# Performance work log

Measured on AMD Instinct MI355X. Metric: run time of the kernel, lower is better.

## Reference

```python
import jax, jax.numpy as jnp
import numpy as np

NEG = -1e4      # BigBird additive mask value
LN_EPS = 1e-12  # BERT-style LayerNorm eps


def _bigbird_forward(xs_pad, mask, Wq, bq, Wk, bk, Wv, bv, Wo, bo, gamma, beta, rand_idx):
    b, n, hsz = xs_pad.shape
    H = rand_idx.shape[0]
    nb = rand_idx.shape[1] + 2          # one rand row per non-edge query block
    BS = n // nb                        # block size
    d = hsz // H
    r = rand_idx.shape[2]
    scale = 1.0 / np.sqrt(d).astype(np.float32)

    mf = mask.reshape(b, n).astype(xs_pad.dtype)   # (b,n) 1=token, 0=pad
    mb = mf.reshape(b, nb, BS)                     # blocked mask

    def proj(W, bias):
        return (xs_pad @ W + bias).reshape(b, n, H, d).transpose(0, 2, 1, 3)

    q = proj(Wq, bq) * scale            # (b,H,n,d)
    k = proj(Wk, bk)
    v = proj(Wv, bv)
    qb = q.reshape(b, H, nb, BS, d)
    kb = k.reshape(b, H, nb, BS, d)
    vb = v.reshape(b, H, nb, BS, d)

    # ---- global rows: first / last query block attend to all keys ----
    def full_row(qi):                   # qi: (b,H,BS,d)
        s = jnp.einsum('bhqd,bhkd->bhqk', qi, k) + (1.0 - mf)[:, None, None, :] * NEG
        return jnp.einsum('bhqk,bhkd->bhqd', jax.nn.softmax(s, axis=-1), v)

    ctx_first = full_row(qb[:, :, 0])
    ctx_last = full_row(qb[:, :, nb - 1])

    # ---- random key/value blocks: per-head, per-query-block gather ----
    hidx = jnp.arange(H)[:, None, None]
    rand_k = kb[:, hidx, rand_idx].reshape(b, H, nb - 2, r * BS, d)
    rand_v = vb[:, hidx, rand_idx].reshape(b, H, nb - 2, r * BS, d)
    rand_m = mb[:, rand_idx].reshape(b, H, nb - 2, r * BS)

    def sparse_row(qi, kc, vc, mc):     # kc:(b,H,K,d), mc:(b,H,K)
        s = jnp.einsum('bhqd,bhkd->bhqk', qi, kc) + (1.0 - mc)[:, :, None, :] * NEG
        return jnp.einsum('bhqk,bhkd->bhqd', jax.nn.softmax(s, axis=-1), vc)

    def gather_blocks(ids, ridx):
        kc = jnp.concatenate([kb[:, :, j] for j in ids] + [rand_k[:, :, ridx]], axis=2)
        vc = jnp.concatenate([vb[:, :, j] for j in ids] + [rand_v[:, :, ridx]], axis=2)
        mc = jnp.concatenate([jnp.broadcast_to(mb[:, None, j], (b, H, BS)) for j in ids]
                             + [rand_m[:, :, ridx]], axis=2)
        return kc, vc, mc

    # second / penultimate query blocks: window + globals + rand
    ctx_second = sparse_row(qb[:, :, 1], *gather_blocks([0, 1, 2, nb - 1], 0))
    ctx_penult = sparse_row(qb[:, :, nb - 2], *gather_blocks([nb - 3, nb - 2, nb - 1, 0], nb - 3))

    # ---- middle rows i in [2, nb-3]: 3-block sliding window + first/last global + r random ----
    nmid = nb - 4
    mid = jnp.arange(2, nb - 2)
    win = mid[:, None] + jnp.arange(-1, 2)[None, :]        # (nmid,3)
    k_win = kb[:, :, win].reshape(b, H, nmid, 3 * BS, d)
    v_win = vb[:, :, win].reshape(b, H, nmid, 3 * BS, d)
    m_win = jnp.broadcast_to(mb[:, win].reshape(b, 1, nmid, 3 * BS), (b, H, nmid, 3 * BS))

    def rep_glob(t):                     # (b,H,BS,...) -> (b,H,nmid,BS,...)
        return jnp.broadcast_to(t[:, :, None], (b, H, nmid) + t.shape[2:])

    k_mid = jnp.concatenate([k_win, rep_glob(kb[:, :, 0]), rep_glob(kb[:, :, nb - 1]),
                             rand_k[:, :, 1:nb - 3]], axis=3)
    v_mid = jnp.concatenate([v_win, rep_glob(vb[:, :, 0]), rep_glob(vb[:, :, nb - 1]),
                             rand_v[:, :, 1:nb - 3]], axis=3)
    m_first = jnp.broadcast_to(mb[:, None, None, 0], (b, H, nmid, BS))
    m_last = jnp.broadcast_to(mb[:, None, None, nb - 1], (b, H, nmid, BS))
    m_mid = jnp.concatenate([m_win, m_first, m_last, rand_m[:, :, 1:nb - 3]], axis=3)

    s_mid = jnp.einsum('bhmqd,bhmkd->bhmqk', qb[:, :, 2:nb - 2], k_mid) \
            + (1.0 - m_mid)[:, :, :, None, :] * NEG
    ctx_mid = jnp.einsum('bhmqk,bhmkd->bhmqd', jax.nn.softmax(s_mid, axis=-1), v_mid)

    ctx = jnp.concatenate([ctx_first[:, :, None], ctx_second[:, :, None], ctx_mid,
                           ctx_penult[:, :, None], ctx_last[:, :, None]], axis=2)
    ctx = ctx.reshape(b, H, n, d).transpose(0, 2, 1, 3).reshape(b, n, hsz)
    ctx = ctx * mf[:, :, None]           # from_mask on output rows

    # BigBirdSelfOutput: dense + residual + LayerNorm (dropout=0 / eval)
    y = ctx @ Wo + bo + xs_pad
    mu = y.mean(-1, keepdims=True)
    var = ((y - mu) ** 2).mean(-1, keepdims=True)
    return (y - mu) * jax.lax.rsqrt(var + LN_EPS) * gamma + beta


def setup_inputs() -> dict:
    key = jax.random.key(0)
    ks = jax.random.split(key, 6)
    B, N, HSZ, H, BS, R = 4, 4096, 1024, 16, 64, 3
    NB = N // BS
    init = lambda k, shp: jax.random.normal(k, shp, dtype=jnp.float32) * 0.02
    return {
        'xs_pad': jax.random.normal(ks[0], (B, N, HSZ), dtype=jnp.float32),
        'mask': jnp.ones((B, 1, N), dtype=jnp.int32),
        'Wq': init(ks[1], (HSZ, HSZ)), 'bq': jnp.zeros((HSZ,), jnp.float32),
        'Wk': init(ks[2], (HSZ, HSZ)), 'bk': jnp.zeros((HSZ,), jnp.float32),
        'Wv': init(ks[3], (HSZ, HSZ)), 'bv': jnp.zeros((HSZ,), jnp.float32),
        'Wo': init(ks[4], (HSZ, HSZ)), 'bo': jnp.zeros((HSZ,), jnp.float32),
        'gamma': jnp.ones((HSZ,), jnp.float32), 'beta': jnp.zeros((HSZ,), jnp.float32),
        'rand_idx': jax.random.randint(ks[5], (H, NB - 2, R), 1, NB - 1).astype(jnp.int32),
    }


def reference(xs_pad, mask, Wq, bq, Wk, bk, Wv, bv, Wo, bo, gamma, beta, rand_idx):
    return _bigbird_forward(xs_pad, mask, Wq, bq, Wk, bk, Wv, bv, Wo, bo, gamma, beta, rand_idx)
```

## Files before the change

kernel.cpp:

```cpp
#include <hip/hip_runtime.h>
#include <hip/hip_bf16.h>

#define B_   4
#define N_   4096
#define HSZ  1024
#define H_   16
#define D_   64
#define NB_  64
#define R_   3
#define M_   (B_*N_)
#define NEGV (-1e4f)

typedef float f32x4 __attribute__((ext_vector_type(4)));
typedef short s16x8 __attribute__((ext_vector_type(8)));
typedef __bf16 b16x8 __attribute__((ext_vector_type(8)));

__device__ __forceinline__ f32x4 mfma16(s16x8 a, s16x8 b, f32x4 c) {
  return __builtin_amdgcn_mfma_f32_16x16x32_bf16(
      __builtin_bit_cast(b16x8, a), __builtin_bit_cast(b16x8, b), c, 0, 0, 0);
}

__device__ __forceinline__ short f2b(float x) {
  __hip_bfloat16 h = __float2bfloat16(x);
  return (short)__builtin_bit_cast(unsigned short, h);
}

__device__ __forceinline__ unsigned pack2(float a, float b) {
  return (unsigned)(unsigned short)f2b(a) |
         ((unsigned)(unsigned short)f2b(b) << 16);
}

__device__ __forceinline__ void gl_lds16(const short* g, short* l) {
  __builtin_amdgcn_global_load_lds(
      (const __attribute__((address_space(1))) unsigned int*)g,
      (__attribute__((address_space(3))) unsigned int*)l, 16, 0, 0);
}

__global__ __launch_bounds__(256) void k_conv(const float* __restrict__ in,
                                              short* __restrict__ out) {
  size_t i = ((size_t)blockIdx.x * 256 + threadIdx.x) * 8;
  float4 a = *(const float4*)&in[i];
  float4 b = *(const float4*)&in[i + 4];
  s16x8 o;
  o[0] = f2b(a.x); o[1] = f2b(a.y); o[2] = f2b(a.z); o[3] = f2b(a.w);
  o[4] = f2b(b.x); o[5] = f2b(b.y); o[6] = f2b(b.z); o[7] = f2b(b.w);
  *(s16x8*)&out[i] = o;
}

__global__ __launch_bounds__(256) void k_wt(const float* __restrict__ Wq,
                                            const float* __restrict__ Wk,
                                            const float* __restrict__ Wv,
                                            const float* __restrict__ Wo,
                                            short* __restrict__ out) {
  const int z = blockIdx.z;
  const float* src = (z == 0) ? Wq : (z == 1) ? Wk : (z == 2) ? Wv : Wo;
  short* dst = out + (size_t)z * HSZ * HSZ;
  __shared__ __align__(16) float t[64][68];
  const int tk = blockIdx.x * 64, tn = blockIdx.y * 64;
  const int tid = threadIdx.x;
#pragma unroll
  for (int r = 0; r < 4; ++r) {
    int c = tid + r * 256;
    int row = c >> 4, seg = c & 15;
    *(float4*)&t[row][seg * 4] =
        *(const float4*)&src[(size_t)(tk + row) * HSZ + tn + seg * 4];
  }
  __syncthreads();
#pragma unroll
  for (int r = 0; r < 2; ++r) {
    int c = tid + r * 256;
    int row = c >> 3, seg = c & 7;
    s16x8 o;
#pragma unroll
    for (int u = 0; u < 8; ++u) o[u] = f2b(t[seg * 8 + u][row]);
    *(s16x8*)&dst[(size_t)(tn + row) * HSZ + tk + seg * 8] = o;
  }
}

__global__ __launch_bounds__(256) void k_attb(const int* __restrict__ mask,
                                              float* __restrict__ attb) {
  int i = blockIdx.x * 256 + threadIdx.x;
  attb[i] = (1.0f - (float)mask[i]) * NEGV;
}

template <int PATH>
__global__ __launch_bounds__(256) void k_gemm(
    const short* __restrict__ A, const short* __restrict__ WT,
    const float* __restrict__ bias0, const float* __restrict__ bias1,
    short* __restrict__ o0, short* __restrict__ o1,
    const float* __restrict__ xs, float* __restrict__ yout) {
  const int z = (PATH == 0) ? blockIdx.z : 0;
  const int wsel = (PATH == 0) ? z : (PATH == 1 ? 2 : 3);
  const short* Bt = WT + (size_t)wsel * HSZ * HSZ;
  const float* bias = (PATH == 0 && z == 1) ? bias1 : bias0;
  short* outb = (PATH == 0 && z == 1) ? o1 : o0;
  const float alpha = (PATH == 0 && z == 0) ? 0.125f : 1.0f;

  __shared__ __align__(16) short a_lds[128][64];
  __shared__ __align__(16) short b_lds[128][64];

  const int tid = threadIdx.x, lane = tid & 63, wave = tid >> 6;
  const int lq = lane & 15, g = lane >> 4;
  const int wm = (wave & 1) * 64, wn = (wave >> 1) * 64;
  const int tm = blockIdx.x * 128, tn = blockIdx.y * 128;

  const int srow = wave * 32 + (lane >> 3);
  const int scol = ((lane & 7) ^ ((lane >> 3) & 7)) * 8;

  f32x4 acc[4][4] = {};

  for (int kt = 0; kt < HSZ; kt += 64) {
    __syncthreads();
#pragma unroll
    for (int u = 0; u < 4; ++u) {
      gl_lds16(&A[(size_t)(tm + srow + u * 8) * HSZ + kt + scol],
               &a_lds[wave * 32 + u * 8][0]);
      gl_lds16(&Bt[(size_t)(tn + srow + u * 8) * HSZ + kt + scol],
               &b_lds[wave * 32 + u * 8][0]);
    }
    __syncthreads();
    const int sw = (lq & 7) << 3;
#pragma unroll
    for (int kk = 0; kk < 2; ++kk) {
      const int ko = (kk * 32 + g * 8) ^ sw;
      s16x8 af[4], bf[4];
#pragma unroll
      for (int i = 0; i < 4; ++i)
        af[i] = *(const s16x8*)&a_lds[wm + i * 16 + lq][ko];
#pragma unroll
      for (int j = 0; j < 4; ++j)
        bf[j] = *(const s16x8*)&b_lds[wn + j * 16 + lq][ko];
#pragma unroll
      for (int i = 0; i < 4; ++i)
#pragma unroll
        for (int j = 0; j < 4; ++j)
          acc[i][j] = (PATH == 1) ? mfma16(af[i], bf[j], acc[i][j])
                                  : mfma16(bf[j], af[i], acc[i][j]);
    }
  }

  if (PATH == 1) {
#pragma unroll
    for (int j = 0; j < 4; ++j) {
      const int col = tn + wn + j * 16 + lq;
      const int hh = col >> 6, dd = col & 63;
      const float bi = bias[col];
#pragma unroll
      for (int i = 0; i < 4; ++i) {
        const int nrow = tm + wm + i * 16 + g * 4;
        const int bb = nrow >> 12, nn = nrow & (N_ - 1);
        uint2 w;
        w.x = pack2(acc[i][j][0] + bi, acc[i][j][1] + bi);
        w.y = pack2(acc[i][j][2] + bi, acc[i][j][3] + bi);
        *(uint2*)&o0[(((size_t)bb * H_ + hh) * D_ + dd) * N_ + nn] = w;
      }
    }
    return;
  }

#pragma unroll
  for (int i = 0; i < 4; ++i) {
    const int row = tm + wm + i * 16 + lq;
#pragma unroll
    for (int j = 0; j < 4; ++j) {
      const int colb = tn + wn + j * 16 + g * 4;
      const float4 bi = *(const float4*)&bias[colb];
      if (PATH == 0) {
        const int bb = row >> 12, nn = row & (N_ - 1);
        const int hh = colb >> 6, dd = colb & 63;
        uint2 w;
        w.x = pack2((acc[i][j][0] + bi.x) * alpha,
                    (acc[i][j][1] + bi.y) * alpha);
        w.y = pack2((acc[i][j][2] + bi.z) * alpha,
                    (acc[i][j][3] + bi.w) * alpha);
        *(uint2*)&outb[(((size_t)bb * H_ + hh) * N_ + nn) * D_ + dd] = w;
      } else {
        const size_t idx = (size_t)row * HSZ + colb;
        const float4 xv = *(const float4*)&xs[idx];
        float4 yv;
        yv.x = acc[i][j][0] + bi.x + xv.x;
        yv.y = acc[i][j][1] + bi.y + xv.y;
        yv.z = acc[i][j][2] + bi.z + xv.z;
        yv.w = acc[i][j][3] + bi.w + xv.w;
        *(float4*)&yout[idx] = yv;
      }
    }
  }
}

__global__ __launch_bounds__(256) void k_attn(
    const short* __restrict__ Q, const short* __restrict__ K,
    const short* __restrict__ VT, const float* __restrict__ attb,
    const int* __restrict__ mask, const int* __restrict__ rnd,
    short* __restrict__ ctx, float* __restrict__ pO,
    float* __restrict__ pm, float* __restrict__ pl) {
  const int s = blockIdx.x, h = blockIdx.y, b = blockIdx.z;
  const int tid = threadIdx.x, lane = tid & 63, wave = tid >> 6;
  const int g = lane >> 4, lq = lane & 15;

  __shared__ __align__(16) short k_lds[64][72];
  __shared__ __align__(16) short vt_lds[64][72];
  __shared__ __align__(16) short p_lds[4][16][72];
  __shared__ __align__(16) float bias_s[64];
  __shared__ int list_s[8];
  __shared__ int Ls;

  const bool mid = (s < 62);
  const int qb = mid ? (s + 1) : (((s - 62) >> 3) ? (NB_ - 1) : 0);

  if (tid == 0) {
    int L;
    if (!mid) {
      int chunk = (s - 62) & 7;
#pragma unroll
      for (int i = 0; i < 8; ++i) list_s[i] = chunk * 8 + i;
      L = 8;
    } else {
      const int* rp = rnd + ((size_t)h * (NB_ - 2) + (qb - 1)) * R_;
      int n;
      if (qb == 1) {
        list_s[0] = 0; list_s[1] = 1; list_s[2] = 2; list_s[3] = NB_ - 1; n = 4;
      } else if (qb == NB_ - 2) {
        list_s[0] = NB_ - 3; list_s[1] = NB_ - 2; list_s[2] = NB_ - 1;
        list_s[3] = 0; n = 4;
      } else {
        list_s[0] = qb - 1; list_s[1] = qb; list_s[2] = qb + 1;
        list_s[3] = 0; list_s[4] = NB_ - 1; n = 5;
      }
      for (int j = 0; j < R_; ++j) list_s[n + j] = rp[j];
      L = n + R_;
    }
    Ls = L;
  }

  const size_t bh = (size_t)b * H_ + h;
  const size_t qrow = bh * N_ + (size_t)qb * 64 + wave * 16 + lq;
  s16x8 qf0 = *(const s16x8*)&Q[qrow * D_ + g * 8];
  s16x8 qf1 = *(const s16x8*)&Q[qrow * D_ + 32 + g * 8];

  __syncthreads();
  const int L = Ls;

  const int r0 = tid >> 3, sg0 = tid & 7;
  const int r1 = 32 + (tid >> 3), sg1 = tid & 7;

  s16x8 kr0, kr1, vr0, vr1;
  float br = 0.0f;
  {
    const int kb = list_s[0];
    const short* kp = &K[(bh * N_ + (size_t)kb * 64) * D_];
    const short* vp = &VT[bh * (size_t)D_ * N_ + (size_t)kb * 64];
    kr0 = *(const s16x8*)&kp[r0 * D_ + sg0 * 8];
    kr1 = *(const s16x8*)&kp[r1 * D_ + sg1 * 8];
    vr0 = *(const s16x8*)&vp[(size_t)r0 * N_ + sg0 * 8];
    vr1 = *(const s16x8*)&vp[(size_t)r1 * N_ + sg1 * 8];
    if (tid < 64) br = attb[(size_t)b * N_ + kb * 64 + tid];
  }

  f32x4 o[4] = {};
  float m_run = -INFINITY, ssum = 0.0f;

  for (int it = 0; it < L; ++it) {
    *(s16x8*)&k_lds[r0][sg0 * 8] = kr0;
    *(s16x8*)&k_lds[r1][sg1 * 8] = kr1;
    *(s16x8*)&vt_lds[r0][sg0 * 8] = vr0;
    *(s16x8*)&vt_lds[r1][sg1 * 8] = vr1;
    if (tid < 64) bias_s[tid] = br;
    if (it + 1 < L) {
      const int kb = list_s[it + 1];
      const short* kp = &K[(bh * N_ + (size_t)kb * 64) * D_];
      const short* vp = &VT[bh * (size_t)D_ * N_ + (size_t)kb * 64];
      kr0 = *(const s16x8*)&kp[r0 * D_ + sg0 * 8];
      kr1 = *(const s16x8*)&kp[r1 * D_ + sg1 * 8];
      vr0 = *(const s16x8*)&vp[(size_t)r0 * N_ + sg0 * 8];
      vr1 = *(const s16x8*)&vp[(size_t)r1 * N_ + sg1 * 8];
      if (tid < 64) br = attb[(size_t)b * N_ + kb * 64 + tid];
    }
    __syncthreads();

    f32x4 st[4];
#pragma unroll
    for (int f = 0; f < 4; ++f) {
      f32x4 acc0 = {};
#pragma unroll
      for (int kk = 0; kk < 2; ++kk) {
        s16x8 af = *(const s16x8*)&k_lds[f * 16 + lq][kk * 32 + g * 8];
        acc0 = mfma16(af, kk ? qf1 : qf0, acc0);
      }
      f32x4 b4 = *(const f32x4*)&bias_s[f * 16 + g * 4];
      st[f] = acc0 + b4;
    }

    float bm = -INFINITY;
#pragma unroll
    for (int f = 0; f < 4; ++f)
#pragma unroll
      for (int e = 0; e < 4; ++e) bm = fmaxf(bm, st[f][e]);
    bm = fmaxf(bm, __shfl_xor(bm, 16));
    bm = fmaxf(bm, __shfl_xor(bm, 32));
    float mnew = fmaxf(m_run, bm);
    float al = __expf(m_run - mnew);
    float psum = 0.0f;
#pragma unroll
    for (int f = 0; f < 4; ++f)
#pragma unroll
      for (int e = 0; e < 4; ++e) {
        float p = __expf(st[f][e] - mnew);
        st[f][e] = p;
        psum += p;
      }
    psum += __shfl_xor(psum, 16);
    psum += __shfl_xor(psum, 32);
    ssum = ssum * al + psum;
    m_run = mnew;

#pragma unroll
    for (int f = 0; f < 4; ++f) {
      uint2 w = make_uint2(pack2(st[f][0], st[f][1]),
                           pack2(st[f][2], st[f][3]));
      *(uint2*)&p_lds[wave][lq][f * 16 + g * 4] = w;
    }

    float a0 = __shfl(al, g * 4 + 0);
    float a1 = __shfl(al, g * 4 + 1);
    float a2 = __shfl(al, g * 4 + 2);
    float a3 = __shfl(al, g * 4 + 3);
#pragma unroll
    for (int j = 0; j < 4; ++j) {
      o[j][0] *= a0; o[j][1] *= a1; o[j][2] *= a2; o[j][3] *= a3;
    }

#pragma unroll
    for (int kk = 0; kk < 2; ++kk) {
      s16x8 pa = *(const s16x8*)&p_lds[wave][lq][kk * 32 + g * 8];
#pragma unroll
      for (int j = 0; j < 4; ++j) {
        s16x8 bv = *(const s16x8*)&vt_lds[j * 16 + lq][kk * 32 + g * 8];
        o[j] = mfma16(pa, bv, o[j]);
      }
    }
    __syncthreads();
  }

  if (mid) {
    float rs = (float)mask[(size_t)b * N_ + qb * 64 + wave * 16 + lq] / ssum;
    float s0 = __shfl(rs, g * 4 + 0);
    float s1 = __shfl(rs, g * 4 + 1);
    float s2 = __shfl(rs, g * 4 + 2);
    float s3 = __shfl(rs, g * 4 + 3);
#pragma unroll
    for (int j = 0; j < 4; ++j) {
      k_lds[wave * 16 + g * 4 + 0][j * 16 + lq] = f2b(o[j][0] * s0);
      k_lds[wave * 16 + g * 4 + 1][j * 16 + lq] = f2b(o[j][1] * s1);
      k_lds[wave * 16 + g * 4 + 2][j * 16 + lq] = f2b(o[j][2] * s2);
      k_lds[wave * 16 + g * 4 + 3][j * 16 + lq] = f2b(o[j][3] * s3);
    }
    __syncthreads();
#pragma unroll
    for (int p = 0; p < 2; ++p) {
      int c = tid + p * 256;
      int row = c >> 3, seg = c & 7;
      *(s16x8*)&ctx[((size_t)b * N_ + qb * 64 + row) * HSZ + h * D_ + seg * 8] =
          *(const s16x8*)&k_lds[row][seg * 8];
    }
  } else {
    const int e2 = s - 62;
    const int qsel = e2 >> 3, chunk = e2 & 7;
    const size_t eidx = (bh * 2 + qsel) * 8 + chunk;
    float* po = pO + eidx * 4096;
#pragma unroll
    for (int j = 0; j < 4; ++j)
#pragma unroll
      for (int e = 0; e < 4; ++e)
        po[(wave * 16 + g * 4 + e) * 64 + j * 16 + lq] = o[j][e];
    if (lane < 16) {
      pm[eidx * 64 + wave * 16 + lane] = m_run;
      pl[eidx * 64 + wave * 16 + lane] = ssum;
    }
  }
}

__global__ __launch_bounds__(256) void k_comb(
    const float* __restrict__ pO, const float* __restrict__ pm,
    const float* __restrict__ pl, const int* __restrict__ mask,
    short* __restrict__ ctx) {
  const int qsel = blockIdx.x, h = blockIdx.y, b = blockIdx.z;
  const int qb = qsel ? NB_ - 1 : 0;
  const int tid = threadIdx.x;
  const int q = tid >> 2, dq = tid & 3;
  const size_t base = (((size_t)b * H_ + h) * 2 + qsel) * 8;

  float mv[8];
  float M = -INFINITY;
#pragma unroll
  for (int i = 0; i < 8; ++i) {
    mv[i] = pm[(base + i) * 64 + q];
    M = fmaxf(M, mv[i]);
  }
  float Lsum = 0.0f;
#pragma unroll
  for (int i = 0; i < 8; ++i) {
    float w = __expf(mv[i] - M);
    mv[i] = w;
    Lsum += pl[(base + i) * 64 + q] * w;
  }
  f32x4 acc[4] = {};
#pragma unroll
  for (int i = 0; i < 8; ++i) {
    const float* p = pO + (base + i) * 4096 + q * 64 + dq * 16;
    float w = mv[i];
#pragma unroll
    for (int u = 0; u < 4; ++u) {
      f32x4 v = *(const f32x4*)&p[u * 4];
      acc[u] += v * w;
    }
  }
  float sc = (float)mask[(size_t)b * N_ + qb * 64 + q] / Lsum;
  s16x8 out0, out1;
#pragma unroll
  for (int u = 0; u < 8; ++u) {
    out0[u] = f2b(acc[u >> 2][u & 3] * sc);
    out1[u] = f2b(acc[2 + (u >> 2)][u & 3] * sc);
  }
  short* dst = &ctx[((size_t)b * N_ + qb * 64 + q) * HSZ + h * D_ + dq * 16];
  *(s16x8*)dst = out0;
  *(s16x8*)(dst + 8) = out1;
}

__global__ __launch_bounds__(256) void k_ln(float* __restrict__ y,
                                            const float* __restrict__ gamma,
                                            const float* __restrict__ beta) {
  const int row = blockIdx.x, tid = threadIdx.x, lane = tid & 63,
            wave = tid >> 6;
  __shared__ float s_sum[4], s_sq[4];
  float4 v = *(const float4*)&y[(size_t)row * HSZ + tid * 4];
  float s = v.x + v.y + v.z + v.w;
  float q = v.x * v.x + v.y * v.y + v.z * v.z + v.w * v.w;
#pragma unroll
  for (int m = 1; m <= 32; m <<= 1) {
    s += __shfl_xor(s, m);
    q += __shfl_xor(q, m);
  }
  if (lane == 0) { s_sum[wave] = s; s_sq[wave] = q; }
  __syncthreads();
  float S = s_sum[0] + s_sum[1] + s_sum[2] + s_sum[3];
  float Qs = s_sq[0] + s_sq[1] + s_sq[2] + s_sq[3];
  float mu = S * (1.0f / HSZ);
  float var = Qs * (1.0f / HSZ) - mu * mu;
  float r = rsqrtf(var + 1e-12f);
  float4 g = *(const float4*)&gamma[tid * 4];
  float4 be = *(const float4*)&beta[tid * 4];
  float4 outv;
  outv.x = (v.x - mu) * r * g.x + be.x;
  outv.y = (v.y - mu) * r * g.y + be.y;
  outv.z = (v.z - mu) * r * g.z + be.z;
  outv.w = (v.w - mu) * r * g.w + be.w;
  *(float4*)&y[(size_t)row * HSZ + tid * 4] = outv;
}

extern "C" void kernel_launch(void* const* d_in, const int* in_sizes, int n_in,
                              void* d_out, int out_size, void* d_ws,
                              size_t ws_size, hipStream_t stream) {
  const float* xs = (const float*)d_in[0];
  const int* mask = (const int*)d_in[1];
  const float* Wq = (const float*)d_in[2];
  const float* bq = (const float*)d_in[3];
  const float* Wk = (const float*)d_in[4];
  const float* bk = (const float*)d_in[5];
  const float* Wv = (const float*)d_in[6];
  const float* bv = (const float*)d_in[7];
  const float* Wo = (const float*)d_in[8];
  const float* bo = (const float*)d_in[9];
  const float* gamma = (const float*)d_in[10];
  const float* beta = (const float*)d_in[11];
  const int* rnd = (const int*)d_in[12];
  float* yout = (float*)d_out;

  char* ws = (char*)d_ws;
  const size_t SZ_XS = (size_t)M_ * HSZ * 2;
  const size_t SZ_WT = (size_t)4 * HSZ * HSZ * 2;
  short* xsb = (short*)ws;
  short* wt = (short*)(ws + SZ_XS);
  short* qbuf = (short*)(ws + SZ_XS + SZ_WT);
  short* kbuf = qbuf + (size_t)M_ * HSZ;
  short* vtb = kbuf + (size_t)M_ * HSZ;
  char* after = ws + SZ_XS + SZ_WT + 3 * SZ_XS;
  float* attb = (float*)after;
  float* pO = (float*)(after + (1 << 20));
  float* pm = pO + (size_t)1024 * 4096;
  float* pl = pm + (size_t)1024 * 64;

  k_conv<<<8192, 256, 0, stream>>>(xs, xsb);
  k_wt<<<dim3(16, 16, 4), 256, 0, stream>>>(Wq, Wk, Wv, Wo, wt);
  k_attb<<<64, 256, 0, stream>>>(mask, attb);
  k_gemm<0><<<dim3(128, 8, 2), 256, 0, stream>>>(
      xsb, wt, bq, bk, qbuf, kbuf, nullptr, nullptr);
  k_gemm<1><<<dim3(128, 8, 1), 256, 0, stream>>>(
      xsb, wt, bv, nullptr, vtb, nullptr, nullptr, nullptr);
  k_attn<<<dim3(78, H_, B_), 256, 0, stream>>>(qbuf, kbuf, vtb, attb, mask,
                                               rnd, xsb, pO, pm, pl);
  k_comb<<<dim3(2, H_, B_), 256, 0, stream>>>(pO, pm, pl, mask, xsb);
  k_gemm<2><<<dim3(128, 8, 1), 256, 0, stream>>>(
      xsb, wt, bo, nullptr, nullptr, nullptr, xs, yout);
  k_ln<<<M_, 256, 0, stream>>>(yout, gamma, beta);
}
```

Baseline: 379.4 us.

## Load attention K/V fragments straight to registers, use exp2 and lazy rescale

```diff
diff --git a/kernel.cpp b/kernel.cpp
--- a/kernel.cpp
+++ b/kernel.cpp
@@ -10,6 +10,7 @@
 #define R_   3
 #define M_   (B_*N_)
 #define NEGV (-1e4f)
+#define LOG2E 1.4426950408889634f
 
 typedef float f32x4 __attribute__((ext_vector_type(4)));
 typedef short s16x8 __attribute__((ext_vector_type(8)));
@@ -80,7 +81,7 @@
 __global__ __launch_bounds__(256) void k_attb(const int* __restrict__ mask,
                                               float* __restrict__ attb) {
   int i = blockIdx.x * 256 + threadIdx.x;
-  attb[i] = (1.0f - (float)mask[i]) * NEGV;
+  attb[i] = (1.0f - (float)mask[i]) * NEGV * LOG2E;
 }
 
 template <int PATH>
@@ -94,7 +95,7 @@
   const short* Bt = WT + (size_t)wsel * HSZ * HSZ;
   const float* bias = (PATH == 0 && z == 1) ? bias1 : bias0;
   short* outb = (PATH == 0 && z == 1) ? o1 : o0;
-  const float alpha = (PATH == 0 && z == 0) ? 0.125f : 1.0f;
+  const float alpha = (PATH == 0 && z == 0) ? 0.125f * LOG2E : 1.0f;
 
   __shared__ __align__(16) short a_lds[128][64];
   __shared__ __align__(16) short b_lds[128][64];
@@ -198,10 +199,7 @@
   const int tid = threadIdx.x, lane = tid & 63, wave = tid >> 6;
   const int g = lane >> 4, lq = lane & 15;
 
-  __shared__ __align__(16) short k_lds[64][72];
-  __shared__ __align__(16) short vt_lds[64][72];
   __shared__ __align__(16) short p_lds[4][16][72];
-  __shared__ __align__(16) float bias_s[64];
   __shared__ int list_s[8];
   __shared__ int Ls;
 
@@ -241,78 +239,84 @@
   __syncthreads();
   const int L = Ls;
 
-  const int r0 = tid >> 3, sg0 = tid & 7;
-  const int r1 = 32 + (tid >> 3), sg1 = tid & 7;
-
-  s16x8 kr0, kr1, vr0, vr1;
-  float br = 0.0f;
-  {
-    const int kb = list_s[0];
-    const short* kp = &K[(bh * N_ + (size_t)kb * 64) * D_];
-    const short* vp = &VT[bh * (size_t)D_ * N_ + (size_t)kb * 64];
-    kr0 = *(const s16x8*)&kp[r0 * D_ + sg0 * 8];
-    kr1 = *(const s16x8*)&kp[r1 * D_ + sg1 * 8];
-    vr0 = *(const s16x8*)&vp[(size_t)r0 * N_ + sg0 * 8];
-    vr1 = *(const s16x8*)&vp[(size_t)r1 * N_ + sg1 * 8];
-    if (tid < 64) br = attb[(size_t)b * N_ + kb * 64 + tid];
-  }
+  const short* Kb = K + bh * (size_t)N_ * D_;
+  const short* Vb = VT + bh * (size_t)D_ * N_;
+  const float* ab = attb + (size_t)b * N_;
 
   f32x4 o[4] = {};
   float m_run = -INFINITY, ssum = 0.0f;
 
+  int kb = list_s[0];
+  s16x8 kr[4][2];
+#pragma unroll
+  for (int f = 0; f < 4; ++f)
+#pragma unroll
+    for (int kk = 0; kk < 2; ++kk)
+      kr[f][kk] = *(const s16x8*)&Kb[(size_t)(kb * 64 + f * 16 + lq) * D_ +
+                                     kk * 32 + g * 8];
+
   for (int it = 0; it < L; ++it) {
-    *(s16x8*)&k_lds[r0][sg0 * 8] = kr0;
-    *(s16x8*)&k_lds[r1][sg1 * 8] = kr1;
-    *(s16x8*)&vt_lds[r0][sg0 * 8] = vr0;
-    *(s16x8*)&vt_lds[r1][sg1 * 8] = vr1;
-    if (tid < 64) bias_s[tid] = br;
+    s16x8 vr[4][2];
+#pragma unroll
+    for (int j = 0; j < 4; ++j)
+#pragma unroll
+      for (int kk = 0; kk < 2; ++kk)
+        vr[j][kk] = *(const s16x8*)&Vb[(size_t)(j * 16 + lq) * N_ + kb * 64 +
+                                       kk * 32 + g * 8];
+
+    f32x4 st[4];
+#pragma unroll
+    for (int f = 0; f < 4; ++f) {
+      f32x4 a0 = {};
+      a0 = mfma16(kr[f][0], qf0, a0);
+      a0 = mfma16(kr[f][1], qf1, a0);
+      f32x4 b4 = *(const f32x4*)&ab[kb * 64 + f * 16 + g * 4];
+      st[f] = a0 + b4;
+    }
+
     if (it + 1 < L) {
-      const int kb = list_s[it + 1];
-      const short* kp = &K[(bh * N_ + (size_t)kb * 64) * D_];
-      const short* vp = &VT[bh * (size_t)D_ * N_ + (size_t)kb * 64];
-      kr0 = *(const s16x8*)&kp[r0 * D_ + sg0 * 8];
-      kr1 = *(const s16x8*)&kp[r1 * D_ + sg1 * 8];
-      vr0 = *(const s16x8*)&vp[(size_t)r0 * N_ + sg0 * 8];
-      vr1 = *(const s16x8*)&vp[(size_t)r1 * N_ + sg1 * 8];
-      if (tid < 64) br = attb[(size_t)b * N_ + kb * 64 + tid];
-    }
-    __syncthreads();
-
-    f32x4 st[4];
-#pragma unroll
-    for (int f = 0; f < 4; ++f) {
-      f32x4 acc0 = {};
-#pragma unroll
-      for (int kk = 0; kk < 2; ++kk) {
-        s16x8 af = *(const s16x8*)&k_lds[f * 16 + lq][kk * 32 + g * 8];
-        acc0 = mfma16(af, kk ? qf1 : qf0, acc0);
-      }
-      f32x4 b4 = *(const f32x4*)&bias_s[f * 16 + g * 4];
-      st[f] = acc0 + b4;
-    }
-
-    float bm = -INFINITY;
-#pragma unroll
-    for (int f = 0; f < 4; ++f)
-#pragma unroll
-      for (int e = 0; e < 4; ++e) bm = fmaxf(bm, st[f][e]);
+      const int kb_nx = list_s[it + 1];
+#pragma unroll
+      for (int f = 0; f < 4; ++f)
+#pragma unroll
+        for (int kk = 0; kk < 2; ++kk)
+          kr[f][kk] = *(const s16x8*)&Kb[(size_t)(kb_nx * 64 + f * 16 + lq) *
+                                             D_ + kk * 32 + g * 8];
+      kb = kb_nx;
+    }
+
+    float t0 = fmaxf(fmaxf(st[0][0], st[0][1]), fmaxf(st[0][2], st[0][3]));
+    float t1 = fmaxf(fmaxf(st[1][0], st[1][1]), fmaxf(st[1][2], st[1][3]));
+    float t2 = fmaxf(fmaxf(st[2][0], st[2][1]), fmaxf(st[2][2], st[2][3]));
+    float t3 = fmaxf(fmaxf(st[3][0], st[3][1]), fmaxf(st[3][2], st[3][3]));
+    float bm = fmaxf(fmaxf(t0, t1), fmaxf(t2, t3));
     bm = fmaxf(bm, __shfl_xor(bm, 16));
     bm = fmaxf(bm, __shfl_xor(bm, 32));
-    float mnew = fmaxf(m_run, bm);
-    float al = __expf(m_run - mnew);
+    if (!__all(bm <= m_run + 8.0f)) {
+      float mnew = fmaxf(m_run, bm);
+      float al = exp2f(m_run - mnew);
+      f32x4 av;
+      av[0] = __shfl(al, g * 4 + 0);
+      av[1] = __shfl(al, g * 4 + 1);
+      av[2] = __shfl(al, g * 4 + 2);
+      av[3] = __shfl(al, g * 4 + 3);
+#pragma unroll
+      for (int j = 0; j < 4; ++j) o[j] *= av;
+      ssum *= al;
+      m_run = mnew;
+    }
     float psum = 0.0f;
 #pragma unroll
     for (int f = 0; f < 4; ++f)
 #pragma unroll
       for (int e = 0; e < 4; ++e) {
-        float p = __expf(st[f][e] - mnew);
+        float p = exp2f(st[f][e] - m_run);
         st[f][e] = p;
         psum += p;
       }
     psum += __shfl_xor(psum, 16);
     psum += __shfl_xor(psum, 32);
-    ssum = ssum * al + psum;
-    m_run = mnew;
+    ssum += psum;
 
 #pragma unroll
     for (int f = 0; f < 4; ++f) {
@@ -321,25 +325,13 @@
       *(uint2*)&p_lds[wave][lq][f * 16 + g * 4] = w;
     }
 
-    float a0 = __shfl(al, g * 4 + 0);
-    float a1 = __shfl(al, g * 4 + 1);
-    float a2 = __shfl(al, g * 4 + 2);
-    float a3 = __shfl(al, g * 4 + 3);
-#pragma unroll
-    for (int j = 0; j < 4; ++j) {
-      o[j][0] *= a0; o[j][1] *= a1; o[j][2] *= a2; o[j][3] *= a3;
-    }
-
 #pragma unroll
     for (int kk = 0; kk < 2; ++kk) {
       s16x8 pa = *(const s16x8*)&p_lds[wave][lq][kk * 32 + g * 8];
 #pragma unroll
-      for (int j = 0; j < 4; ++j) {
-        s16x8 bv = *(const s16x8*)&vt_lds[j * 16 + lq][kk * 32 + g * 8];
-        o[j] = mfma16(pa, bv, o[j]);
-      }
-    }
-    __syncthreads();
+      for (int j = 0; j < 4; ++j)
+        o[j] = mfma16(pa, vr[j][kk], o[j]);
+    }
   }
 
   if (mid) {
@@ -348,12 +340,13 @@
     float s1 = __shfl(rs, g * 4 + 1);
     float s2 = __shfl(rs, g * 4 + 2);
     float s3 = __shfl(rs, g * 4 + 3);
+    short (*ost)[72] = reinterpret_cast<short(*)[72]>(&p_lds[0][0][0]);
 #pragma unroll
     for (int j = 0; j < 4; ++j) {
-      k_lds[wave * 16 + g * 4 + 0][j * 16 + lq] = f2b(o[j][0] * s0);
-      k_lds[wave * 16 + g * 4 + 1][j * 16 + lq] = f2b(o[j][1] * s1);
-      k_lds[wave * 16 + g * 4 + 2][j * 16 + lq] = f2b(o[j][2] * s2);
-      k_lds[wave * 16 + g * 4 + 3][j * 16 + lq] = f2b(o[j][3] * s3);
+      ost[wave * 16 + g * 4 + 0][j * 16 + lq] = f2b(o[j][0] * s0);
+      ost[wave * 16 + g * 4 + 1][j * 16 + lq] = f2b(o[j][1] * s1);
+      ost[wave * 16 + g * 4 + 2][j * 16 + lq] = f2b(o[j][2] * s2);
+      ost[wave * 16 + g * 4 + 3][j * 16 + lq] = f2b(o[j][3] * s3);
     }
     __syncthreads();
 #pragma unroll
@@ -361,7 +354,7 @@
       int c = tid + p * 256;
       int row = c >> 3, seg = c & 7;
       *(s16x8*)&ctx[((size_t)b * N_ + qb * 64 + row) * HSZ + h * D_ + seg * 8] =
-          *(const s16x8*)&k_lds[row][seg * 8];
+          *(const s16x8*)&ost[row][seg * 8];
     }
   } else {
     const int e2 = s - 62;
@@ -400,7 +393,7 @@
   float Lsum = 0.0f;
 #pragma unroll
   for (int i = 0; i < 8; ++i) {
-    float w = __expf(mv[i] - M);
+    float w = exp2f(mv[i] - M);
     mv[i] = w;
     Lsum += pl[(base + i) * 64 + q] * w;
   }
```

Result: slower. 582.2 us (+53.5%).
